# Optimization experiments

Hardware: AMD Instinct MI355X
Metric: run time of the kernel (lower is better)

## Reference

```python
import jax, jax.numpy as jnp
import numpy as np

TOTAL = 819200   # total flattened labels
BATCH = 16384    # number of samples (segments)
DIM = 128        # embed_dim
LABELS_PER = 50  # constant segment length (TOTAL = BATCH * LABELS_PER)


def setup_inputs() -> dict:
    key = jax.random.key(0)
    k_emb, k_w1, k_b1, k_w2, k_b2 = jax.random.split(key, 5)
    embeddings = jax.random.normal(k_emb, (TOTAL, DIM), dtype=jnp.float32)
    # weight_net params (PyTorch nn.Linear default-ish init scale)
    s1 = 1.0 / np.sqrt(DIM)
    W1 = jax.random.uniform(k_w1, (DIM, DIM), jnp.float32, -s1, s1)
    b1 = jax.random.uniform(k_b1, (DIM,), jnp.float32, -s1, s1)
    W2 = jax.random.uniform(k_w2, (DIM, 1), jnp.float32, -s1, s1)
    b2 = jax.random.uniform(k_b2, (1,), jnp.float32, -s1, s1)
    lengths = jnp.full((BATCH,), LABELS_PER, dtype=jnp.int32)
    return {"embeddings": embeddings, "W1": W1, "b1": b1, "W2": W2, "b2": b2,
            "lengths": lengths}


def reference(embeddings, W1, b1, W2, b2, lengths):
    # MLP scorer: Linear -> ReLU -> Linear -> Softmax(dim=0) (GLOBAL over all labels)
    h = jnp.maximum(embeddings @ W1 + b1, 0.0)           # (T, D)
    scores = h @ W2 + b2                                  # (T, 1)
    weights = jax.nn.softmax(scores, axis=0)              # (T, 1) global softmax
    # Ragged per-segment weighted sum via segment_sum
    batch = lengths.shape[0]
    total = embeddings.shape[0]
    seg_ids = jnp.repeat(jnp.arange(batch, dtype=jnp.int32), lengths,
                         total_repeat_length=total)       # (T,)
    pooled = jax.ops.segment_sum(embeddings * weights, seg_ids,
                                 num_segments=batch)      # (B, D)
    return pooled
```

## Files before the change

kernel.cpp:

```cpp
#include <hip/hip_runtime.h>
#include <hip/hip_bf16.h>
#include <math.h>

#define DIM 128

typedef __attribute__((ext_vector_type(8))) short bf16x8;
typedef __attribute__((ext_vector_type(4))) float f32x4;

union FragU { bf16x8 v; __hip_bfloat162 h[4]; };

static __device__ __forceinline__ ushort f2bf(float f) {
    unsigned u = __float_as_uint(f);
    u += 0x7FFFu + ((u >> 16) & 1u);
    return (ushort)(u >> 16);
}

typedef __attribute__((address_space(1))) const unsigned GASp;
typedef __attribute__((address_space(3))) unsigned LASp;
static __device__ __forceinline__ void gll16(const void* g, void* l) {
    __builtin_amdgcn_global_load_lds((GASp*)g, (LASp*)l, 16, 0, 0);
}

static __device__ __forceinline__ void stage16(float* buf, const float* emb,
                                               long row0, long Tm1, int lane) {
    #pragma unroll
    for (int i = 0; i < 8; ++i) {
        int s = i * 64 + lane;
        int r = s >> 5, x = s & 31;
        long gr = row0 + r; gr = (gr > Tm1) ? Tm1 : gr;
        gll16(emb + gr * 128 + ((x ^ (r & 7)) << 2), (char*)buf + i * 1024);
    }
}

__global__ __launch_bounds__(1024) void scan_kernel(const int* __restrict__ lengths,
                                                    int* __restrict__ offsets, int batch) {
    __shared__ int tsum[1024];
    int tid = threadIdx.x;
    int per = (batch + 1023) >> 10;
    int start = tid * per;
    int s = 0;
    for (int i = 0; i < per; ++i) {
        int idx = start + i;
        if (idx < batch) s += lengths[idx];
    }
    tsum[tid] = s;
    __syncthreads();
    for (int off = 1; off < 1024; off <<= 1) {
        int v = (tid >= off) ? tsum[tid - off] : 0;
        __syncthreads();
        tsum[tid] += v;
        __syncthreads();
    }
    int base = (tid == 0) ? 0 : tsum[tid - 1];
    for (int i = 0; i < per; ++i) {
        int idx = start + i;
        if (idx < batch) { offsets[idx] = base; base += lengths[idx]; }
    }
}

__global__ __launch_bounds__(256, 2) void fused_kernel(
        const float* __restrict__ emb, const float* __restrict__ W1,
        const float* __restrict__ b1, const float* __restrict__ W2,
        const float* __restrict__ b2, const int* __restrict__ offsets,
        const int* __restrict__ lengths, int batch, int T,
        float* __restrict__ mArr, float* __restrict__ sArr,
        float* __restrict__ tvec) {
    __shared__ __align__(16) char smem[65536];

    int tid = threadIdx.x;
    int lane = tid & 63;
    int wv = tid >> 6;
    int lr = lane & 15;
    int lg = lane >> 4;

    ushort* sB = (ushort*)smem;
    for (int i = 0; i < 16; ++i) {
        int q = tid + i * 256;
        int n = q >> 5;
        int k4 = q & 31;
        ushort4 w;
        w.x = f2bf(W1[(k4 * 4 + 0) * DIM + n]);
        w.y = f2bf(W1[(k4 * 4 + 1) * DIM + n]);
        w.z = f2bf(W1[(k4 * 4 + 2) * DIM + n]);
        w.w = f2bf(W1[(k4 * 4 + 3) * DIM + n]);
        int c = k4 >> 1;
        int a16 = n * 128 + ((c ^ (n & 7)) * 8) + (k4 & 1) * 4;
        *(ushort4*)&sB[a16] = w;
    }
    __syncthreads();
    bf16x8 bfrag[8][4];
    #pragma unroll
    for (int ct = 0; ct < 8; ++ct) {
        int n = ct * 16 + lr;
        #pragma unroll
        for (int kc = 0; kc < 4; ++kc) {
            int c = lg + kc * 4;
            bfrag[ct][kc] = *(const bf16x8*)&sB[n * 128 + ((c ^ (n & 7)) * 8)];
        }
    }
    float b1reg[8], w2reg[8];
    #pragma unroll
    for (int ct = 0; ct < 8; ++ct) {
        b1reg[ct] = b1[ct * 16 + lr];
        w2reg[ct] = W2[ct * 16 + lr];
    }
    __syncthreads();

    float* buf0 = (float*)(smem + wv * 16384);
    float* buf1 = (float*)(smem + wv * 16384 + 8192);

    long Tm1 = (long)T - 1;
    int nwaves = gridDim.x * 4;
    int gwave = blockIdx.x * 4 + wv;
    int per = (batch + nwaves - 1) / nwaves;
    int seg0 = gwave * per;
    int segend = seg0 + per; if (segend > batch) segend = batch;

    int xc = lane >> 1, xh = lane & 1;

    for (int seg = seg0; seg < segend; ++seg) {
        long off = offsets[seg];
        int len = lengths[seg];
        int nch = (len + 15) >> 4;
        float r_ref = -INFINITY, Sp = 0.f, t0 = 0.f, t1 = 0.f;

        if (nch > 0) stage16(buf0, emb, off, Tm1, lane);
        if (nch > 1) stage16(buf1, emb, off + 16, Tm1, lane);

        for (int c = 0; c < nch; ++c) {
            float* bufc = (c & 1) ? buf1 : buf0;
            if (c + 1 < nch) asm volatile("s_waitcnt vmcnt(8)" ::: "memory");
            else             asm volatile("s_waitcnt vmcnt(0)" ::: "memory");

            bf16x8 a[4];
            #pragma unroll
            for (int kc = 0; kc < 4; ++kc) {
                int c0 = kc * 8 + lg * 2;
                float4 q0 = *(const float4*)&bufc[(lr * 32 + (c0 ^ (lr & 7))) * 4];
                float4 q1 = *(const float4*)&bufc[(lr * 32 + ((c0 + 1) ^ (lr & 7))) * 4];
                FragU f;
                f.h[0] = __float22bfloat162_rn(make_float2(q0.x, q0.y));
                f.h[1] = __float22bfloat162_rn(make_float2(q0.z, q0.w));
                f.h[2] = __float22bfloat162_rn(make_float2(q1.x, q1.y));
                f.h[3] = __float22bfloat162_rn(make_float2(q1.z, q1.w));
                a[kc] = f.v;
            }

            f32x4 acc[8];
            #pragma unroll
            for (int ct = 0; ct < 8; ++ct) acc[ct] = (f32x4)(0.f);
            #pragma unroll
            for (int ct = 0; ct < 8; ++ct)
                #pragma unroll
                for (int kc = 0; kc < 4; ++kc)
                    acc[ct] = __builtin_amdgcn_mfma_f32_16x16x32_bf16(a[kc], bfrag[ct][kc], acc[ct], 0, 0, 0);

            float p[4];
            #pragma unroll
            for (int reg = 0; reg < 4; ++reg) {
                float s = 0.f;
                #pragma unroll
                for (int ct = 0; ct < 8; ++ct) {
                    float h = acc[ct][reg] + b1reg[ct];
                    h = fmaxf(h, 0.f);
                    s = fmaf(h, w2reg[ct], s);
                }
                p[reg] = s;
            }
            #pragma unroll
            for (int m = 1; m < 16; m <<= 1) {
                #pragma unroll
                for (int reg = 0; reg < 4; ++reg)
                    p[reg] += __shfl_xor(p[reg], m, 64);
            }
            int r3 = lane & 3;
            float pr = p[0];
            pr = (r3 == 1) ? p[1] : pr;
            pr = (r3 == 2) ? p[2] : pr;
            pr = (r3 == 3) ? p[3] : pr;
            int src = ((lane & 12) << 2) + r3;
            float sv = __shfl(pr, src, 64);

            int cv = len - c * 16;
            float s_l = (lr < cv) ? sv : -INFINITY;

            if (!__all(s_l - r_ref <= 8.f)) {
                float m_c = s_l;
                #pragma unroll
                for (int o = 1; o < 16; o <<= 1) m_c = fmaxf(m_c, __shfl_xor(m_c, o, 64));
                float r_new = fmaxf(r_ref, m_c);
                float scl = __expf(r_ref - r_new);
                Sp *= scl; t0 *= scl; t1 *= scl;
                r_ref = r_new;
            }
            float w_l = __expf(s_l - r_ref);
            Sp += w_l;

            #pragma unroll
            for (int jg = 0; jg < 4; ++jg) {
                int j0 = jg * 4;
                float2 e0 = *(const float2*)&bufc[((j0 + 0) * 32 + (xc ^ ((j0 + 0) & 7))) * 4 + xh * 2];
                float2 e1 = *(const float2*)&bufc[((j0 + 1) * 32 + (xc ^ ((j0 + 1) & 7))) * 4 + xh * 2];
                float2 e2 = *(const float2*)&bufc[((j0 + 2) * 32 + (xc ^ ((j0 + 2) & 7))) * 4 + xh * 2];
                float2 e3 = *(const float2*)&bufc[((j0 + 3) * 32 + (xc ^ ((j0 + 3) & 7))) * 4 + xh * 2];
                float w0 = __uint_as_float(__builtin_amdgcn_readlane(__float_as_uint(w_l), j0 + 0));
                float w1v = __uint_as_float(__builtin_amdgcn_readlane(__float_as_uint(w_l), j0 + 1));
                float w2v = __uint_as_float(__builtin_amdgcn_readlane(__float_as_uint(w_l), j0 + 2));
                float w3 = __uint_as_float(__builtin_amdgcn_readlane(__float_as_uint(w_l), j0 + 3));
                t0 = fmaf(w0, e0.x, t0); t1 = fmaf(w0, e0.y, t1);
                t0 = fmaf(w1v, e1.x, t0); t1 = fmaf(w1v, e1.y, t1);
                t0 = fmaf(w2v, e2.x, t0); t1 = fmaf(w2v, e2.y, t1);
                t0 = fmaf(w3, e3.x, t0); t1 = fmaf(w3, e3.y, t1);
            }

            asm volatile("s_waitcnt lgkmcnt(0)" ::: "memory");
            if (c + 2 < nch) stage16(bufc, emb, off + (long)(c + 2) * 16, Tm1, lane);
        }

        #pragma unroll
        for (int o = 1; o < 16; o <<= 1) Sp += __shfl_xor(Sp, o, 64);
        *(float2*)&tvec[(long)seg * DIM + 2 * lane] = make_float2(t0, t1);
        if (lane == 0) { mArr[seg] = r_ref; sArr[seg] = Sp; }
    }
}

__global__ __launch_bounds__(1024) void segreduce_kernel(const float* __restrict__ mArr,
        const float* __restrict__ sArr, int batch, float* __restrict__ stats) {
    __shared__ float redm[16], reds[16];
    int tid = threadIdx.x;
    int wave = tid >> 6, ln = tid & 63;
    float m = -INFINITY;
    for (int i = tid; i < batch; i += 1024) m = fmaxf(m, mArr[i]);
    #pragma unroll
    for (int o = 32; o >= 1; o >>= 1) m = fmaxf(m, __shfl_xor(m, o, 64));
    if (ln == 0) redm[wave] = m;
    __syncthreads();
    float M = -INFINITY;
    #pragma unroll
    for (int k = 0; k < 16; ++k) M = fmaxf(M, redm[k]);
    float s = 0.f;
    for (int i = tid; i < batch; i += 1024) s += sArr[i] * expf(mArr[i] - M);
    #pragma unroll
    for (int o = 32; o >= 1; o >>= 1) s += __shfl_xor(s, o, 64);
    if (ln == 0) reds[wave] = s;
    __syncthreads();
    if (tid == 0) {
        float S = 0.f;
        #pragma unroll
        for (int k = 0; k < 16; ++k) S += reds[k];
        stats[0] = M;
        stats[1] = 1.0f / S;
    }
}

__global__ __launch_bounds__(256) void scale_kernel(const float* __restrict__ tvec,
        const float* __restrict__ mArr, const float* __restrict__ stats,
        float* __restrict__ out, int n) {
    int idx = blockIdx.x * 256 + threadIdx.x;
    if (idx >= n) return;
    float M = stats[0], invS = stats[1];
    int b = idx >> 7;
    out[idx] = tvec[idx] * (expf(mArr[b] - M) * invS);
}

extern "C" void kernel_launch(void* const* d_in, const int* in_sizes, int n_in,
                              void* d_out, int out_size, void* d_ws, size_t ws_size,
                              hipStream_t stream) {
    const float* emb     = (const float*)d_in[0];
    const float* W1      = (const float*)d_in[1];
    const float* b1      = (const float*)d_in[2];
    const float* W2      = (const float*)d_in[3];
    const float* b2      = (const float*)d_in[4];
    const int*   lengths = (const int*)d_in[5];
    int T = in_sizes[0] / DIM;
    int batch = in_sizes[5];
    float* out = (float*)d_out;

    int*   offsets = (int*)d_ws;
    float* mArr    = (float*)(offsets + batch);
    float* sArr    = mArr + batch;
    float* stats   = sArr + batch;
    float* tvec    = stats + 2;

    scan_kernel<<<1, 1024, 0, stream>>>(lengths, offsets, batch);
    fused_kernel<<<512, 256, 0, stream>>>(emb, W1, b1, W2, b2, offsets, lengths,
                                          batch, T, mArr, sArr, tvec);
    segreduce_kernel<<<1, 1024, 0, stream>>>(mArr, sArr, batch, stats);
    scale_kernel<<<(out_size + 255) / 256, 256, 0, stream>>>(tvec, mArr, stats, out, out_size);
}
```

Measured before the change: 164.7 us.

## Stream contiguous row range per wave across segment boundaries instead of per-segment chunks

Each wave now processes the whole contiguous row range of its assigned segments as one stream of 16-row chunks, splitting chunks at segment boundaries inside the loop. Before, every segment of 50 rows was padded to 4 chunks (64 rows), wasting MFMA work and loads on masked rows and restarting the prefetch pipeline per segment. The change adds a boundary-splitting inner loop with a scalar per-row fallback for partial chunks, plus extra divergent control flow and the online-softmax rescale per sub-range.

```diff
diff --git a/kernel.cpp b/kernel.cpp
--- a/kernel.cpp
+++ b/kernel.cpp
@@ -115,74 +115,85 @@
     int per = (batch + nwaves - 1) / nwaves;
     int seg0 = gwave * per;
     int segend = seg0 + per; if (segend > batch) segend = batch;
+    if (seg0 >= segend) return;
+
+    long row0 = offsets[seg0];
+    long rowend = (segend < batch) ? (long)offsets[segend] : (long)T;
+    int nch = (int)((rowend - row0 + 15) >> 4);
 
     int xc = lane >> 1, xh = lane & 1;
 
-    for (int seg = seg0; seg < segend; ++seg) {
-        long off = offsets[seg];
-        int len = lengths[seg];
-        int nch = (len + 15) >> 4;
-        float r_ref = -INFINITY, Sp = 0.f, t0 = 0.f, t1 = 0.f;
-
-        if (nch > 0) stage16(buf0, emb, off, Tm1, lane);
-        if (nch > 1) stage16(buf1, emb, off + 16, Tm1, lane);
-
-        for (int c = 0; c < nch; ++c) {
-            float* bufc = (c & 1) ? buf1 : buf0;
-            if (c + 1 < nch) asm volatile("s_waitcnt vmcnt(8)" ::: "memory");
-            else             asm volatile("s_waitcnt vmcnt(0)" ::: "memory");
-
-            bf16x8 a[4];
+    int seg = seg0;
+    int bnd = lengths[seg];
+    float r_ref = -INFINITY, Sp = 0.f, t0 = 0.f, t1 = 0.f;
+
+    if (nch > 0) stage16(buf0, emb, row0, Tm1, lane);
+    if (nch > 1) stage16(buf1, emb, row0 + 16, Tm1, lane);
+
+    for (int c = 0; c < nch; ++c) {
+        float* bufc = (c & 1) ? buf1 : buf0;
+        if (c + 1 < nch) asm volatile("s_waitcnt vmcnt(8)" ::: "memory");
+        else             asm volatile("s_waitcnt vmcnt(0)" ::: "memory");
+
+        bf16x8 a[4];
+        #pragma unroll
+        for (int kc = 0; kc < 4; ++kc) {
+            int c0 = kc * 8 + lg * 2;
+            float4 q0 = *(const float4*)&bufc[(lr * 32 + (c0 ^ (lr & 7))) * 4];
+            float4 q1 = *(const float4*)&bufc[(lr * 32 + ((c0 + 1) ^ (lr & 7))) * 4];
+            FragU f;
+            f.h[0] = __float22bfloat162_rn(make_float2(q0.x, q0.y));
+            f.h[1] = __float22bfloat162_rn(make_float2(q0.z, q0.w));
+            f.h[2] = __float22bfloat162_rn(make_float2(q1.x, q1.y));
+            f.h[3] = __float22bfloat162_rn(make_float2(q1.z, q1.w));
+            a[kc] = f.v;
+        }
+
+        f32x4 acc[8];
+        #pragma unroll
+        for (int ct = 0; ct < 8; ++ct) acc[ct] = (f32x4)(0.f);
+        #pragma unroll
+        for (int ct = 0; ct < 8; ++ct)
             #pragma unroll
-            for (int kc = 0; kc < 4; ++kc) {
-                int c0 = kc * 8 + lg * 2;
-                float4 q0 = *(const float4*)&bufc[(lr * 32 + (c0 ^ (lr & 7))) * 4];
-                float4 q1 = *(const float4*)&bufc[(lr * 32 + ((c0 + 1) ^ (lr & 7))) * 4];
-                FragU f;
-                f.h[0] = __float22bfloat162_rn(make_float2(q0.x, q0.y));
-                f.h[1] = __float22bfloat162_rn(make_float2(q0.z, q0.w));
-                f.h[2] = __float22bfloat162_rn(make_float2(q1.x, q1.y));
-                f.h[3] = __float22bfloat162_rn(make_float2(q1.z, q1.w));
-                a[kc] = f.v;
+            for (int kc = 0; kc < 4; ++kc)
+                acc[ct] = __builtin_amdgcn_mfma_f32_16x16x32_bf16(a[kc], bfrag[ct][kc], acc[ct], 0, 0, 0);
+
+        float p[4];
+        #pragma unroll
+        for (int reg = 0; reg < 4; ++reg) {
+            float s = 0.f;
+            #pragma unroll
+            for (int ct = 0; ct < 8; ++ct) {
+                float h = acc[ct][reg] + b1reg[ct];
+                h = fmaxf(h, 0.f);
+                s = fmaf(h, w2reg[ct], s);
             }
-
-            f32x4 acc[8];
+            p[reg] = s;
+        }
+        #pragma unroll
+        for (int m = 1; m < 16; m <<= 1) {
             #pragma unroll
-            for (int ct = 0; ct < 8; ++ct) acc[ct] = (f32x4)(0.f);
-            #pragma unroll
-            for (int ct = 0; ct < 8; ++ct)
-                #pragma unroll
-                for (int kc = 0; kc < 4; ++kc)
-                    acc[ct] = __builtin_amdgcn_mfma_f32_16x16x32_bf16(a[kc], bfrag[ct][kc], acc[ct], 0, 0, 0);
-
-            float p[4];
-            #pragma unroll
-            for (int reg = 0; reg < 4; ++reg) {
-                float s = 0.f;
-                #pragma unroll
-                for (int ct = 0; ct < 8; ++ct) {
-                    float h = acc[ct][reg] + b1reg[ct];
-                    h = fmaxf(h, 0.f);
-                    s = fmaf(h, w2reg[ct], s);
-                }
-                p[reg] = s;
-            }
-            #pragma unroll
-            for (int m = 1; m < 16; m <<= 1) {
-                #pragma unroll
-                for (int reg = 0; reg < 4; ++reg)
-                    p[reg] += __shfl_xor(p[reg], m, 64);
-            }
-            int r3 = lane & 3;
-            float pr = p[0];
-            pr = (r3 == 1) ? p[1] : pr;
-            pr = (r3 == 2) ? p[2] : pr;
-            pr = (r3 == 3) ? p[3] : pr;
-            int src = ((lane & 12) << 2) + r3;
-            float sv = __shfl(pr, src, 64);
-
-            int cv = len - c * 16;
-            float s_l = (lr < cv) ? sv : -INFINITY;
+            for (int reg = 0; reg < 4; ++reg)
+                p[reg] += __shfl_xor(p[reg], m, 64);
+        }
+        int r3 = lane & 3;
+        float pr = p[0];
+        pr = (r3 == 1) ? p[1] : pr;
+        pr = (r3 == 2) ? p[2] : pr;
+        pr = (r3 == 3) ? p[3] : pr;
+        int src = ((lane & 12) << 2) + r3;
+        float sv = __shfl(pr, src, 64);
+
+        int vrows = (int)(rowend - (row0 + (long)c * 16));
+        if (vrows > 16) vrows = 16;
+        float s_all = (lr < vrows) ? sv : -INFINITY;
+
+        int pos = 0;
+        while (pos < vrows) {
+            int take = vrows - pos;
+            if (take > bnd) take = bnd;
+            int end = pos + take;
+            float s_l = (lr >= pos && lr < end) ? s_all : -INFINITY;
 
             if (!__all(s_l - r_ref <= 8.f)) {
                 float m_c = s_l;
@@ -196,31 +207,49 @@
             float w_l = __expf(s_l - r_ref);
             Sp += w_l;
 
-            #pragma unroll
-            for (int jg = 0; jg < 4; ++jg) {
-                int j0 = jg * 4;
-                float2 e0 = *(const float2*)&bufc[((j0 + 0) * 32 + (xc ^ ((j0 + 0) & 7))) * 4 + xh * 2];
-                float2 e1 = *(const float2*)&bufc[((j0 + 1) * 32 + (xc ^ ((j0 + 1) & 7))) * 4 + xh * 2];
-                float2 e2 = *(const float2*)&bufc[((j0 + 2) * 32 + (xc ^ ((j0 + 2) & 7))) * 4 + xh * 2];
-                float2 e3 = *(const float2*)&bufc[((j0 + 3) * 32 + (xc ^ ((j0 + 3) & 7))) * 4 + xh * 2];
-                float w0 = __uint_as_float(__builtin_amdgcn_readlane(__float_as_uint(w_l), j0 + 0));
-                float w1v = __uint_as_float(__builtin_amdgcn_readlane(__float_as_uint(w_l), j0 + 1));
-                float w2v = __uint_as_float(__builtin_amdgcn_readlane(__float_as_uint(w_l), j0 + 2));
-                float w3 = __uint_as_float(__builtin_amdgcn_readlane(__float_as_uint(w_l), j0 + 3));
-                t0 = fmaf(w0, e0.x, t0); t1 = fmaf(w0, e0.y, t1);
-                t0 = fmaf(w1v, e1.x, t0); t1 = fmaf(w1v, e1.y, t1);
-                t0 = fmaf(w2v, e2.x, t0); t1 = fmaf(w2v, e2.y, t1);
-                t0 = fmaf(w3, e3.x, t0); t1 = fmaf(w3, e3.y, t1);
+            if (pos == 0 && end == 16) {
+                #pragma unroll
+                for (int jg = 0; jg < 4; ++jg) {
+                    int j0 = jg * 4;
+                    float2 e0 = *(const float2*)&bufc[((j0 + 0) * 32 + (xc ^ ((j0 + 0) & 7))) * 4 + xh * 2];
+                    float2 e1 = *(const float2*)&bufc[((j0 + 1) * 32 + (xc ^ ((j0 + 1) & 7))) * 4 + xh * 2];
+                    float2 e2 = *(const float2*)&bufc[((j0 + 2) * 32 + (xc ^ ((j0 + 2) & 7))) * 4 + xh * 2];
+                    float2 e3 = *(const float2*)&bufc[((j0 + 3) * 32 + (xc ^ ((j0 + 3) & 7))) * 4 + xh * 2];
+                    float w0 = __uint_as_float(__builtin_amdgcn_readlane(__float_as_uint(w_l), j0 + 0));
+                    float w1v = __uint_as_float(__builtin_amdgcn_readlane(__float_as_uint(w_l), j0 + 1));
+                    float w2v = __uint_as_float(__builtin_amdgcn_readlane(__float_as_uint(w_l), j0 + 2));
+                    float w3 = __uint_as_float(__builtin_amdgcn_readlane(__float_as_uint(w_l), j0 + 3));
+                    t0 = fmaf(w0, e0.x, t0); t1 = fmaf(w0, e0.y, t1);
+                    t0 = fmaf(w1v, e1.x, t0); t1 = fmaf(w1v, e1.y, t1);
+                    t0 = fmaf(w2v, e2.x, t0); t1 = fmaf(w2v, e2.y, t1);
+                    t0 = fmaf(w3, e3.x, t0); t1 = fmaf(w3, e3.y, t1);
+                }
+            } else {
+                for (int j = pos; j < end; ++j) {
+                    float wj = __uint_as_float(__builtin_amdgcn_readlane(__float_as_uint(w_l), j));
+                    float2 e = *(const float2*)&bufc[(j * 32 + (xc ^ (j & 7))) * 4 + xh * 2];
+                    t0 = fmaf(wj, e.x, t0);
+                    t1 = fmaf(wj, e.y, t1);
+                }
             }
 
-            asm volatile("s_waitcnt lgkmcnt(0)" ::: "memory");
-            if (c + 2 < nch) stage16(bufc, emb, off + (long)(c + 2) * 16, Tm1, lane);
-        }
-
-        #pragma unroll
-        for (int o = 1; o < 16; o <<= 1) Sp += __shfl_xor(Sp, o, 64);
-        *(float2*)&tvec[(long)seg * DIM + 2 * lane] = make_float2(t0, t1);
-        if (lane == 0) { mArr[seg] = r_ref; sArr[seg] = Sp; }
+            bnd -= take;
+            pos = end;
+            if (bnd == 0) {
+                float Ssum = Sp;
+                #pragma unroll
+                for (int o = 1; o < 16; o <<= 1) Ssum += __shfl_xor(Ssum, o, 64);
+                *(float2*)&tvec[(long)seg * DIM + 2 * lane] = make_float2(t0, t1);
+                if (lane == 0) { mArr[seg] = r_ref; sArr[seg] = Ssum; }
+                r_ref = -INFINITY; Sp = 0.f; t0 = 0.f; t1 = 0.f;
+                ++seg;
+                if (seg >= segend) break;
+                bnd = lengths[seg];
+            }
+        }
+
+        asm volatile("s_waitcnt lgkmcnt(0)" ::: "memory");
+        if (c + 2 < nch) stage16(bufc, emb, row0 + (long)(c + 2) * 16, Tm1, lane);
     }
 }
 
```

Measured after the change: 176.7 us. 1.07x slower.

## Pipeline chunk prefetch across segments when all segment lengths are equal

Applied to the files above, without the earlier changes.

The scan kernel now checks whether every segment has the same length and writes a flag. When the flag is set, the fused kernel computes offsets as seg*L and keeps the double-buffered async loads running across segment boundaries, so the next segment's first chunks are prefetched while the current one finishes. Previously each segment drained the pipeline and restarted it, leaving load latency exposed. The general path is kept as a fallback for ragged lengths, at the cost of some extra code and an extra flag read.

```diff
diff --git a/kernel.cpp b/kernel.cpp
--- a/kernel.cpp
+++ b/kernel.cpp
@@ -33,18 +33,28 @@
 }
 
 __global__ __launch_bounds__(1024) void scan_kernel(const int* __restrict__ lengths,
-                                                    int* __restrict__ offsets, int batch) {
+                                                    int* __restrict__ offsets, int batch,
+                                                    int* __restrict__ uniflag) {
     __shared__ int tsum[1024];
+    __shared__ int ok;
     int tid = threadIdx.x;
+    if (tid == 0) ok = 1;
+    int L0 = lengths[0];
     int per = (batch + 1023) >> 10;
     int start = tid * per;
     int s = 0;
+    int loc = 1;
     for (int i = 0; i < per; ++i) {
         int idx = start + i;
-        if (idx < batch) s += lengths[idx];
+        if (idx < batch) {
+            int l = lengths[idx];
+            s += l;
+            if (l != L0) loc = 0;
+        }
     }
     tsum[tid] = s;
     __syncthreads();
+    if (!loc) atomicAnd(&ok, 0);
     for (int off = 1; off < 1024; off <<= 1) {
         int v = (tid >= off) ? tsum[tid - off] : 0;
         __syncthreads();
@@ -56,6 +66,94 @@
         int idx = start + i;
         if (idx < batch) { offsets[idx] = base; base += lengths[idx]; }
     }
+    __syncthreads();
+    if (tid == 0) uniflag[0] = ok;
+}
+
+static __device__ __forceinline__ void chunk_body(
+        const float* __restrict__ bufc, int cv, int lane, int lr, int lg,
+        int xc, int xh, const bf16x8 (&bfrag)[8][4],
+        const float (&b1r)[8], const float (&w2r)[8],
+        float& r_ref, float& Sp, float& t0, float& t1) {
+    bf16x8 a[4];
+    #pragma unroll
+    for (int kc = 0; kc < 4; ++kc) {
+        int c0 = kc * 8 + lg * 2;
+        float4 q0 = *(const float4*)&bufc[(lr * 32 + (c0 ^ (lr & 7))) * 4];
+        float4 q1 = *(const float4*)&bufc[(lr * 32 + ((c0 + 1) ^ (lr & 7))) * 4];
+        FragU f;
+        f.h[0] = __float22bfloat162_rn(make_float2(q0.x, q0.y));
+        f.h[1] = __float22bfloat162_rn(make_float2(q0.z, q0.w));
+        f.h[2] = __float22bfloat162_rn(make_float2(q1.x, q1.y));
+        f.h[3] = __float22bfloat162_rn(make_float2(q1.z, q1.w));
+        a[kc] = f.v;
+    }
+
+    f32x4 acc[8];
+    #pragma unroll
+    for (int ct = 0; ct < 8; ++ct) acc[ct] = (f32x4)(0.f);
+    #pragma unroll
+    for (int ct = 0; ct < 8; ++ct)
+        #pragma unroll
+        for (int kc = 0; kc < 4; ++kc)
+            acc[ct] = __builtin_amdgcn_mfma_f32_16x16x32_bf16(a[kc], bfrag[ct][kc], acc[ct], 0, 0, 0);
+
+    float p[4];
+    #pragma unroll
+    for (int reg = 0; reg < 4; ++reg) {
+        float s = 0.f;
+        #pragma unroll
+        for (int ct = 0; ct < 8; ++ct) {
+            float h = acc[ct][reg] + b1r[ct];
+            h = fmaxf(h, 0.f);
+            s = fmaf(h, w2r[ct], s);
+        }
+        p[reg] = s;
+    }
+    #pragma unroll
+    for (int m = 1; m < 16; m <<= 1) {
+        #pragma unroll
+        for (int reg = 0; reg < 4; ++reg)
+            p[reg] += __shfl_xor(p[reg], m, 64);
+    }
+    int r3 = lane & 3;
+    float pr = p[0];
+    pr = (r3 == 1) ? p[1] : pr;
+    pr = (r3 == 2) ? p[2] : pr;
+    pr = (r3 == 3) ? p[3] : pr;
+    int src = ((lane & 12) << 2) + r3;
+    float sv = __shfl(pr, src, 64);
+
+    float s_l = (lr < cv) ? sv : -INFINITY;
+
+    if (!__all(s_l - r_ref <= 8.f)) {
+        float m_c = s_l;
+        #pragma unroll
+        for (int o = 1; o < 16; o <<= 1) m_c = fmaxf(m_c, __shfl_xor(m_c, o, 64));
+        float r_new = fmaxf(r_ref, m_c);
+        float scl = __expf(r_ref - r_new);
+        Sp *= scl; t0 *= scl; t1 *= scl;
+        r_ref = r_new;
+    }
+    float w_l = __expf(s_l - r_ref);
+    Sp += w_l;
+
+    #pragma unroll
+    for (int jg = 0; jg < 4; ++jg) {
+        int j0 = jg * 4;
+        float2 e0 = *(const float2*)&bufc[((j0 + 0) * 32 + (xc ^ ((j0 + 0) & 7))) * 4 + xh * 2];
+        float2 e1 = *(const float2*)&bufc[((j0 + 1) * 32 + (xc ^ ((j0 + 1) & 7))) * 4 + xh * 2];
+        float2 e2 = *(const float2*)&bufc[((j0 + 2) * 32 + (xc ^ ((j0 + 2) & 7))) * 4 + xh * 2];
+        float2 e3 = *(const float2*)&bufc[((j0 + 3) * 32 + (xc ^ ((j0 + 3) & 7))) * 4 + xh * 2];
+        float w0 = __uint_as_float(__builtin_amdgcn_readlane(__float_as_uint(w_l), j0 + 0));
+        float w1v = __uint_as_float(__builtin_amdgcn_readlane(__float_as_uint(w_l), j0 + 1));
+        float w2v = __uint_as_float(__builtin_amdgcn_readlane(__float_as_uint(w_l), j0 + 2));
+        float w3 = __uint_as_float(__builtin_amdgcn_readlane(__float_as_uint(w_l), j0 + 3));
+        t0 = fmaf(w0, e0.x, t0); t1 = fmaf(w0, e0.y, t1);
+        t0 = fmaf(w1v, e1.x, t0); t1 = fmaf(w1v, e1.y, t1);
+        t0 = fmaf(w2v, e2.x, t0); t1 = fmaf(w2v, e2.y, t1);
+        t0 = fmaf(w3, e3.x, t0); t1 = fmaf(w3, e3.y, t1);
+    }
 }
 
 __global__ __launch_bounds__(256, 2) void fused_kernel(
@@ -63,6 +161,7 @@
         const float* __restrict__ b1, const float* __restrict__ W2,
         const float* __restrict__ b2, const int* __restrict__ offsets,
         const int* __restrict__ lengths, int batch, int T,
+        const int* __restrict__ uniflag,
         float* __restrict__ mArr, float* __restrict__ sArr,
         float* __restrict__ tvec) {
     __shared__ __align__(16) char smem[65536];
@@ -98,11 +197,11 @@
             bfrag[ct][kc] = *(const bf16x8*)&sB[n * 128 + ((c ^ (n & 7)) * 8)];
         }
     }
-    float b1reg[8], w2reg[8];
+    float b1r[8], w2r[8];
     #pragma unroll
     for (int ct = 0; ct < 8; ++ct) {
-        b1reg[ct] = b1[ct * 16 + lr];
-        w2reg[ct] = W2[ct * 16 + lr];
+        b1r[ct] = b1[ct * 16 + lr];
+        w2r[ct] = W2[ct * 16 + lr];
     }
     __syncthreads();
 
@@ -115,112 +214,69 @@
     int per = (batch + nwaves - 1) / nwaves;
     int seg0 = gwave * per;
     int segend = seg0 + per; if (segend > batch) segend = batch;
+    if (seg0 >= segend) return;
 
     int xc = lane >> 1, xh = lane & 1;
-
-    for (int seg = seg0; seg < segend; ++seg) {
-        long off = offsets[seg];
-        int len = lengths[seg];
-        int nch = (len + 15) >> 4;
-        float r_ref = -INFINITY, Sp = 0.f, t0 = 0.f, t1 = 0.f;
-
-        if (nch > 0) stage16(buf0, emb, off, Tm1, lane);
-        if (nch > 1) stage16(buf1, emb, off + 16, Tm1, lane);
-
-        for (int c = 0; c < nch; ++c) {
-            float* bufc = (c & 1) ? buf1 : buf0;
-            if (c + 1 < nch) asm volatile("s_waitcnt vmcnt(8)" ::: "memory");
-            else             asm volatile("s_waitcnt vmcnt(0)" ::: "memory");
-
-            bf16x8 a[4];
-            #pragma unroll
-            for (int kc = 0; kc < 4; ++kc) {
-                int c0 = kc * 8 + lg * 2;
-                float4 q0 = *(const float4*)&bufc[(lr * 32 + (c0 ^ (lr & 7))) * 4];
-                float4 q1 = *(const float4*)&bufc[(lr * 32 + ((c0 + 1) ^ (lr & 7))) * 4];
-                FragU f;
-                f.h[0] = __float22bfloat162_rn(make_float2(q0.x, q0.y));
-                f.h[1] = __float22bfloat162_rn(make_float2(q0.z, q0.w));
-                f.h[2] = __float22bfloat162_rn(make_float2(q1.x, q1.y));
-                f.h[3] = __float22bfloat162_rn(make_float2(q1.z, q1.w));
-                a[kc] = f.v;
+    int uni = __builtin_amdgcn_readfirstlane(uniflag[0]);
+
+    if (uni) {
+        int L = __builtin_amdgcn_readfirstlane(lengths[0]);
+        int nch = (L + 15) >> 4;
+        int ss = seg0, sc = 0;
+        #pragma unroll
+        for (int k = 0; k < 2; ++k) {
+            if (ss < segend) {
+                stage16(k ? buf1 : buf0, emb, (long)ss * L + sc * 16, Tm1, lane);
+                if (++sc == nch) { sc = 0; ++ss; }
             }
-
-            f32x4 acc[8];
-            #pragma unroll
-            for (int ct = 0; ct < 8; ++ct) acc[ct] = (f32x4)(0.f);
-            #pragma unroll
-            for (int ct = 0; ct < 8; ++ct)
-                #pragma unroll
-                for (int kc = 0; kc < 4; ++kc)
-                    acc[ct] = __builtin_amdgcn_mfma_f32_16x16x32_bf16(a[kc], bfrag[ct][kc], acc[ct], 0, 0, 0);
-
-            float p[4];
-            #pragma unroll
-            for (int reg = 0; reg < 4; ++reg) {
-                float s = 0.f;
-                #pragma unroll
-                for (int ct = 0; ct < 8; ++ct) {
-                    float h = acc[ct][reg] + b1reg[ct];
-                    h = fmaxf(h, 0.f);
-                    s = fmaf(h, w2reg[ct], s);
+        }
+        int cur = 0;
+        for (int seg = seg0; seg < segend; ++seg) {
+            float r_ref = -INFINITY, Sp = 0.f, t0 = 0.f, t1 = 0.f;
+            for (int c = 0; c < nch; ++c) {
+                if (seg == segend - 1 && c == nch - 1)
+                    asm volatile("s_waitcnt vmcnt(0)" ::: "memory");
+                else
+                    asm volatile("s_waitcnt vmcnt(8)" ::: "memory");
+                float* bufc = cur ? buf1 : buf0;
+                chunk_body(bufc, L - c * 16, lane, lr, lg, xc, xh,
+                           bfrag, b1r, w2r, r_ref, Sp, t0, t1);
+                asm volatile("s_waitcnt lgkmcnt(0)" ::: "memory");
+                if (ss < segend) {
+                    stage16(bufc, emb, (long)ss * L + sc * 16, Tm1, lane);
+                    if (++sc == nch) { sc = 0; ++ss; }
                 }
-                p[reg] = s;
+                cur ^= 1;
             }
             #pragma unroll
-            for (int m = 1; m < 16; m <<= 1) {
-                #pragma unroll
-                for (int reg = 0; reg < 4; ++reg)
-                    p[reg] += __shfl_xor(p[reg], m, 64);
+            for (int o = 1; o < 16; o <<= 1) Sp += __shfl_xor(Sp, o, 64);
+            *(float2*)&tvec[(long)seg * DIM + 2 * lane] = make_float2(t0, t1);
+            if (lane == 0) { mArr[seg] = r_ref; sArr[seg] = Sp; }
+        }
+    } else {
+        for (int seg = seg0; seg < segend; ++seg) {
+            long off = offsets[seg];
+            int len = lengths[seg];
+            int nch = (len + 15) >> 4;
+            float r_ref = -INFINITY, Sp = 0.f, t0 = 0.f, t1 = 0.f;
+
+            if (nch > 0) stage16(buf0, emb, off, Tm1, lane);
+            if (nch > 1) stage16(buf1, emb, off + 16, Tm1, lane);
+
+            for (int c = 0; c < nch; ++c) {
+                float* bufc = (c & 1) ? buf1 : buf0;
+                if (c + 1 < nch) asm volatile("s_waitcnt vmcnt(8)" ::: "memory");
+                else             asm volatile("s_waitcnt vmcnt(0)" ::: "memory");
+                chunk_body(bufc, len - c * 16, lane, lr, lg, xc, xh,
+                           bfrag, b1r, w2r, r_ref, Sp, t0, t1);
+                asm volatile("s_waitcnt lgkmcnt(0)" ::: "memory");
+                if (c + 2 < nch) stage16(bufc, emb, off + (long)(c + 2) * 16, Tm1, lane);
             }
-            int r3 = lane & 3;
-            float pr = p[0];
-            pr = (r3 == 1) ? p[1] : pr;
-            pr = (r3 == 2) ? p[2] : pr;
-            pr = (r3 == 3) ? p[3] : pr;
-            int src = ((lane & 12) << 2) + r3;
-            float sv = __shfl(pr, src, 64);
-
-            int cv = len - c * 16;
-            float s_l = (lr < cv) ? sv : -INFINITY;
-
-            if (!__all(s_l - r_ref <= 8.f)) {
-                float m_c = s_l;
-                #pragma unroll
-                for (int o = 1; o < 16; o <<= 1) m_c = fmaxf(m_c, __shfl_xor(m_c, o, 64));
-                float r_new = fmaxf(r_ref, m_c);
-                float scl = __expf(r_ref - r_new);
-                Sp *= scl; t0 *= scl; t1 *= scl;
-                r_ref = r_new;
-            }
-            float w_l = __expf(s_l - r_ref);
-            Sp += w_l;
-
             #pragma unroll
-            for (int jg = 0; jg < 4; ++jg) {
-                int j0 = jg * 4;
-                float2 e0 = *(const float2*)&bufc[((j0 + 0) * 32 + (xc ^ ((j0 + 0) & 7))) * 4 + xh * 2];
-                float2 e1 = *(const float2*)&bufc[((j0 + 1) * 32 + (xc ^ ((j0 + 1) & 7))) * 4 + xh * 2];
-                float2 e2 = *(const float2*)&bufc[((j0 + 2) * 32 + (xc ^ ((j0 + 2) & 7))) * 4 + xh * 2];
-                float2 e3 = *(const float2*)&bufc[((j0 + 3) * 32 + (xc ^ ((j0 + 3) & 7))) * 4 + xh * 2];
-                float w0 = __uint_as_float(__builtin_amdgcn_readlane(__float_as_uint(w_l), j0 + 0));
-                float w1v = __uint_as_float(__builtin_amdgcn_readlane(__float_as_uint(w_l), j0 + 1));
-                float w2v = __uint_as_float(__builtin_amdgcn_readlane(__float_as_uint(w_l), j0 + 2));
-                float w3 = __uint_as_float(__builtin_amdgcn_readlane(__float_as_uint(w_l), j0 + 3));
-                t0 = fmaf(w0, e0.x, t0); t1 = fmaf(w0, e0.y, t1);
-                t0 = fmaf(w1v, e1.x, t0); t1 = fmaf(w1v, e1.y, t1);
-                t0 = fmaf(w2v, e2.x, t0); t1 = fmaf(w2v, e2.y, t1);
-                t0 = fmaf(w3, e3.x, t0); t1 = fmaf(w3, e3.y, t1);
-            }
-
-            asm volatile("s_waitcnt lgkmcnt(0)" ::: "memory");
-            if (c + 2 < nch) stage16(bufc, emb, off + (long)(c + 2) * 16, Tm1, lane);
-        }
-
-        #pragma unroll
-        for (int o = 1; o < 16; o <<= 1) Sp += __shfl_xor(Sp, o, 64);
-        *(float2*)&tvec[(long)seg * DIM + 2 * lane] = make_float2(t0, t1);
-        if (lane == 0) { mArr[seg] = r_ref; sArr[seg] = Sp; }
+            for (int o = 1; o < 16; o <<= 1) Sp += __shfl_xor(Sp, o, 64);
+            *(float2*)&tvec[(long)seg * DIM + 2 * lane] = make_float2(t0, t1);
+            if (lane == 0) { mArr[seg] = r_ref; sArr[seg] = Sp; }
+        }
     }
 }
 
@@ -280,11 +336,12 @@
     float* mArr    = (float*)(offsets + batch);
     float* sArr    = mArr + batch;
     float* stats   = sArr + batch;
-    float* tvec    = stats + 2;
-
-    scan_kernel<<<1, 1024, 0, stream>>>(lengths, offsets, batch);
+    int*   uniflag = (int*)(stats + 2);
+    float* tvec    = stats + 4;
+
+    scan_kernel<<<1, 1024, 0, stream>>>(lengths, offsets, batch, uniflag);
     fused_kernel<<<512, 256, 0, stream>>>(emb, W1, b1, W2, b2, offsets, lengths,
-                                          batch, T, mArr, sArr, tvec);
+                                          batch, T, uniflag, mArr, sArr, tvec);
     segreduce_kernel<<<1, 1024, 0, stream>>>(mArr, sArr, batch, stats);
     scale_kernel<<<(out_size + 255) / 256, 256, 0, stream>>>(tvec, mArr, stats, out, out_size);
 }
```

Measured after the change: 163.6 us, median of 3. About the same (-0.7%).
